# Kernel optimization log

Hardware: AMD Instinct MI355X
Metric: run time of the kernel (lower is better)

## Reference

```python
import jax, jax.numpy as jnp
import numpy as np

D = 1024       # d_model
H = 16         # num_heads
DK = D // H    # head dim (64)
DFF = 4096     # SwiGLU hidden dim
THETA = 10000.0
EPS = 1e-5
B, S = 2, 2048


def setup_inputs() -> dict:
    key = jax.random.key(0)
    ks = jax.random.split(key, 9)
    p = lambda k, shape: jax.random.normal(k, shape, dtype=jnp.float32) * 0.02
    return {
        "x": jax.random.normal(ks[0], (B, S, D), dtype=jnp.float32),
        "w_q": p(ks[1], (D, D)),   # Linear stores [out, in]
        "w_k": p(ks[2], (D, D)),
        "w_v": p(ks[3], (D, D)),
        "w_o": p(ks[4], (D, D)),
        "ln1_w": jnp.ones((D,), dtype=jnp.float32),
        "ln2_w": jnp.ones((D,), dtype=jnp.float32),
        "w1": p(ks[5], (DFF, D)),  # gate-in proj: d_model -> dff
        "w2": p(ks[6], (D, DFF)),  # down proj:    dff -> d_model
        "w3": p(ks[7], (DFF, D)),  # up proj:      d_model -> dff
    }


def _rmsnorm(x, w):
    xf = x.astype(jnp.float32)
    inv = jax.lax.rsqrt(jnp.mean(xf * xf, axis=-1, keepdims=True) + EPS)
    return (inv * xf * w).astype(x.dtype)


def _rope(x, pos):
    # x: [..., seq, DK]; pos: [seq]
    inv_freq = THETA ** (-(jnp.arange(0, DK, 2, dtype=jnp.float32) / DK))  # [DK/2]
    ang = pos.astype(jnp.float32)[:, None] * inv_freq                      # [seq, DK/2]
    cos, sin = jnp.cos(ang), jnp.sin(ang)
    xe, xo = x[..., ::2], x[..., 1::2]
    re = cos * xe - sin * xo
    ro = sin * xe + cos * xo
    return jnp.stack((re, ro), axis=-1).reshape(x.shape)  # interleave even/odd


def reference(x, w_q, w_k, w_v, w_o, ln1_w, ln2_w, w1, w2, w3):
    b, s, d = x.shape
    pos = jnp.arange(s)

    # --- attention sublayer ---
    h = _rmsnorm(x, ln1_w)
    def proj(w):  # [b,s,d] x [d,d] -> [b,H,s,DK]
        return jnp.einsum('bsd,ed->bse', h, w).reshape(b, s, H, DK).transpose(0, 2, 1, 3)
    q = _rope(proj(w_q), pos)
    k = _rope(proj(w_k), pos)
    v = proj(w_v)

    scores = jnp.einsum('bhqd,bhkd->bhqk', q, k) / (DK ** 0.5)
    causal = jnp.tril(jnp.ones((s, s), dtype=bool))
    scores = jnp.where(causal, scores, -jnp.inf)
    attn = jax.nn.softmax(scores, axis=-1)
    o = jnp.einsum('bhqk,bhkd->bhqd', attn, v).transpose(0, 2, 1, 3).reshape(b, s, d)
    x = x + jnp.einsum('bsd,ed->bse', o, w_o)

    # --- SwiGLU FFN sublayer ---
    h2 = _rmsnorm(x, ln2_w)
    u = jnp.einsum('bsd,fd->bsf', h2, w1)
    g = jnp.einsum('bsd,fd->bsf', h2, w3)
    ffn = jnp.einsum('bsf,df->bsd', u * jax.nn.sigmoid(u) * g, w2)
    return x + ffn
```

## Files before the change

### kernel.cpp

```cpp
#include <hip/hip_runtime.h>

typedef _Float16 half_t;
typedef _Float16 f16x8 __attribute__((ext_vector_type(8)));
typedef _Float16 f16x4 __attribute__((ext_vector_type(4)));
typedef _Float16 f16x2 __attribute__((ext_vector_type(2)));
typedef float fx4 __attribute__((ext_vector_type(4)));

typedef __attribute__((address_space(1))) const unsigned int as1_cuint;
typedef __attribute__((address_space(3))) unsigned int as3_uint;

__device__ __forceinline__ void gld16(const void* g, void* l) {
    __builtin_amdgcn_global_load_lds((as1_cuint*)g, (as3_uint*)l, 16, 0, 0);
}

#define L256(buf, half, sec) (lbase + (buf) * 65536 + (half) * 16384 + (sec) * 8192)

#define KT256(CUR)                                                            \
  {                                                                           \
    const int BO = (CUR) * 65536;                                             \
    const int st1 = (t < nt - 1), st2 = (t < nt - 2);                         \
    const int s1 = (t + 1) * 128, s2 = (t + 2) * 128;                         \
    f16x8 aLo[4][2], aHi[4][2], bA[2][2], bB[2][2];                           \
                                         \
    _Pragma("unroll") for (int mi = 0; mi < 4; mi++) {                        \
        aLo[mi][0] = *(const f16x8*)(aBase + BO + mi * 2048 + swz0);          \
        aLo[mi][1] = *(const f16x8*)(aBase + BO + mi * 2048 + swz1);          \
    }                                                                         \
    _Pragma("unroll") for (int ni = 0; ni < 2; ni++) {                        \
        bA[ni][0] = *(const f16x8*)(bBase + BO + ni * 2048 + swz0);           \
        bA[ni][1] = *(const f16x8*)(bBase + BO + ni * 2048 + swz1);           \
    }                                                                         \
    if (st1) { gld16(pB10 + s1, L256(1 - (CUR), 3, 0));                       \
               gld16(pB1h + s1, L256(1 - (CUR), 3, 1)); }                     \
    asm volatile("s_waitcnt lgkmcnt(8)" ::: "memory");                        \
    __builtin_amdgcn_s_barrier();                                             \
    asm volatile("s_waitcnt lgkmcnt(0)" ::: "memory");                        \
    __builtin_amdgcn_sched_barrier(0);                                        \
    __builtin_amdgcn_s_setprio(1);                                            \
    _Pragma("unroll") for (int kk = 0; kk < 2; kk++)                          \
      _Pragma("unroll") for (int mi = 0; mi < 4; mi++)                        \
        _Pragma("unroll") for (int ni = 0; ni < 2; ni++)                      \
          acc[mi][ni] = __builtin_amdgcn_mfma_f32_16x16x32_f16(aLo[mi][kk], bA[ni][kk], acc[mi][ni], 0, 0, 0); \
    __builtin_amdgcn_s_setprio(0);                                            \
    __builtin_amdgcn_s_barrier();                                             \
                                         \
    _Pragma("unroll") for (int ni = 0; ni < 2; ni++) {                        \
        bB[ni][0] = *(const f16x8*)(bBase + BO + (2 + ni) * 2048 + swz0);     \
        bB[ni][1] = *(const f16x8*)(bBase + BO + (2 + ni) * 2048 + swz1);     \
    }                                                                         \
    if (st2) { gld16(pA00 + s2, L256(CUR, 0, 0)); }                           \
    __builtin_amdgcn_s_barrier();                                             \
    asm volatile("s_waitcnt lgkmcnt(0)" ::: "memory");                        \
    __builtin_amdgcn_sched_barrier(0);                                        \
    __builtin_amdgcn_s_setprio(1);                                            \
    _Pragma("unroll") for (int kk = 0; kk < 2; kk++)                          \
      _Pragma("unroll") for (int mi = 0; mi < 4; mi++)                        \
        _Pragma("unroll") for (int ni = 0; ni < 2; ni++)                      \
          acc[mi][2 + ni] = __builtin_amdgcn_mfma_f32_16x16x32_f16(aLo[mi][kk], bB[ni][kk], acc[mi][2 + ni], 0, 0, 0); \
    __builtin_amdgcn_s_setprio(0);                                            \
    __builtin_amdgcn_s_barrier();                                             \
                                         \
    _Pragma("unroll") for (int mi = 0; mi < 4; mi++) {                        \
        aHi[mi][0] = *(const f16x8*)(aBase + BO + (4 + mi) * 2048 + swz0);    \
        aHi[mi][1] = *(const f16x8*)(aBase + BO + (4 + mi) * 2048 + swz1);    \
    }                                                                         \
    if (st2) { gld16(pB00 + s2, L256(CUR, 2, 0));                             \
               gld16(pB0h + s2, L256(CUR, 2, 1)); }                           \
    __builtin_amdgcn_s_barrier();                                             \
    asm volatile("s_waitcnt lgkmcnt(0)" ::: "memory");                        \
    __builtin_amdgcn_sched_barrier(0);                                        \
    __builtin_amdgcn_s_setprio(1);                                            \
    _Pragma("unroll") for (int kk = 0; kk < 2; kk++)                          \
      _Pragma("unroll") for (int mi = 0; mi < 4; mi++)                        \
        _Pragma("unroll") for (int ni = 0; ni < 2; ni++)                      \
          acc[4 + mi][2 + ni] = __builtin_amdgcn_mfma_f32_16x16x32_f16(aHi[mi][kk], bB[ni][kk], acc[4 + mi][2 + ni], 0, 0, 0); \
    __builtin_amdgcn_s_setprio(0);                                            \
    __builtin_amdgcn_s_barrier();                                             \
                                         \
    if (st2) { gld16(pA0h + s2, L256(CUR, 0, 1));                             \
               gld16(pA10 + s2, L256(CUR, 1, 0));                             \
               gld16(pA1h + s2, L256(CUR, 1, 1)); }                           \
    __builtin_amdgcn_s_barrier();                                             \
    __builtin_amdgcn_sched_barrier(0);                                        \
    __builtin_amdgcn_s_setprio(1);                                            \
    _Pragma("unroll") for (int kk = 0; kk < 2; kk++)                          \
      _Pragma("unroll") for (int mi = 0; mi < 4; mi++)                        \
        _Pragma("unroll") for (int ni = 0; ni < 2; ni++)                      \
          acc[4 + mi][ni] = __builtin_amdgcn_mfma_f32_16x16x32_f16(aHi[mi][kk], bA[ni][kk], acc[4 + mi][ni], 0, 0, 0); \
    __builtin_amdgcn_s_setprio(0);                                            \
    if (t < nt - 2)       { asm volatile("s_waitcnt vmcnt(6)" ::: "memory"); }\
    else if (t == nt - 2) { asm volatile("s_waitcnt vmcnt(0)" ::: "memory"); }\
    __builtin_amdgcn_s_barrier();                                             \
  }

template<int MODE>
__global__ __launch_bounds__(512, 2)
void gemm256(const half_t* __restrict__ A,
             const half_t* __restrict__ B0, const half_t* __restrict__ B1,
             const half_t* __restrict__ B2,
             half_t* o0, half_t* o1, half_t* o2, half_t* o3,
             int M, int N, int K)
{
    __shared__ half_t smem[65536];
    const int tid = threadIdx.x;
    const int wid = tid >> 6, lane = tid & 63;
    const int lm = lane & 15, lg = lane >> 4;
    const int wr = wid >> 2, wc = wid & 3;
    const int m0 = blockIdx.x * 256, n0 = blockIdx.y * 256;

    const half_t* Bp = B0;
    half_t* outb = o0;
    if (MODE == 1) {
        if (blockIdx.z == 1) { Bp = B1; outb = o1; }
        else if (blockIdx.z == 2) { Bp = B2; outb = o2; }
    }
    if (MODE == 4) {
        if (blockIdx.z == 1) outb = o1;
        else if (blockIdx.z == 2) outb = o2;
        else if (blockIdx.z == 3) outb = o3;
    }
    int Keff = K, koff = 0;
    if (MODE == 4) { Keff = K / gridDim.z; koff = blockIdx.z * Keff; }
    const int nt = Keff >> 6;

    const size_t KB = (size_t)K * 2;
    const int srow = tid >> 3;
    const int schunk = (tid & 7) ^ (srow & 7);
    const char* pA = (const char*)A + (size_t)(m0 + srow) * KB + (size_t)koff * 2 + schunk * 16;
    const char* pB = (const char*)Bp + (size_t)(n0 + srow) * KB + (size_t)koff * 2 + schunk * 16;
    const char* pA00 = pA;
    const char* pA0h = pA + 64 * KB;
    const char* pA10 = pA + 128 * KB;
    const char* pA1h = pA + 192 * KB;
    const char* pB00 = pB;
    const char* pB0h = pB + 64 * KB;
    const char* pB10 = pB + 128 * KB;
    const char* pB1h = pB + 192 * KB;

    char* const lbase = (char*)smem + tid * 16;

    const int swz0 = ((lg ^ (lm & 7)) << 4);
    const int swz1 = (((4 + lg) ^ (lm & 7)) << 4);
    const char* aBase = (const char*)smem + wr * 16384 + lm * 128;
    const char* bBase = (const char*)smem + (2 + (wc >> 1)) * 16384 + (wc & 1) * 8192 + lm * 128;

    gld16(pA00, L256(0, 0, 0));
    gld16(pB00, L256(0, 2, 0)); gld16(pB0h, L256(0, 2, 1));
    gld16(pA0h, L256(0, 0, 1)); gld16(pA10, L256(0, 1, 0)); gld16(pA1h, L256(0, 1, 1));
    gld16(pB10, L256(0, 3, 0)); gld16(pB1h, L256(0, 3, 1));
    gld16(pA00 + 128, L256(1, 0, 0));
    gld16(pB00 + 128, L256(1, 2, 0)); gld16(pB0h + 128, L256(1, 2, 1));
    gld16(pA0h + 128, L256(1, 0, 1)); gld16(pA10 + 128, L256(1, 1, 0)); gld16(pA1h + 128, L256(1, 1, 1));
    asm volatile("s_waitcnt vmcnt(6)" ::: "memory");
    __builtin_amdgcn_s_barrier();

    fx4 acc[8][4] = {};

#pragma unroll 1
    for (int tt = 0; tt < nt; tt += 2) {
        { const int t = tt;     KT256(0) }
        { const int t = tt + 1; KT256(1) }
    }

#pragma unroll
    for (int mi = 0; mi < 8; mi++) {
#pragma unroll
        for (int ni = 0; ni < 4; ni++) {
#pragma unroll
            for (int r = 0; r < 4; r++) {
                int m = m0 + wr * 128 + mi * 16 + lg * 4 + r;
                int n = n0 + wc * 64 + ni * 16 + lm;
                float v = acc[mi][ni][r];
                if (MODE == 1) {
                    int b = m >> 11, s = m & 2047, hh = n >> 6, dk = n & 63;
                    if (blockIdx.z == 2) {
                        outb[((size_t)(b * 16 + hh) * 64 + dk) * 2048 + s] = (half_t)v;
                    } else {
                        outb[((size_t)(b * 16 + hh) * 2048 + s) * 64 + dk] = (half_t)v;
                    }
                } else {
                    outb[(size_t)m * N + n] = (half_t)v;
                }
            }
        }
    }
}

__global__ __launch_bounds__(512, 2)
void gemm_dual9(const half_t* __restrict__ A,
                const half_t* __restrict__ B1, const half_t* __restrict__ B2,
                half_t* __restrict__ out, int M, int N, int K)
{
    __shared__ half_t smem[65536];
    const int tid = threadIdx.x;
    const int wid = tid >> 6, lane = tid & 63;
    const int lm = lane & 15, lg = lane >> 4;
    const int wr = wid >> 2, wc = wid & 3;
    const int m0 = blockIdx.x * 256, n0 = blockIdx.y * 128;

    const size_t KB = (size_t)K * 2;
    const int srow = tid >> 3;
    const int schunk = (tid & 7) ^ (srow & 7);
    const char* pA  = (const char*)A  + (size_t)(m0 + srow) * KB + schunk * 16;
    const char* pB0 = (const char*)B1 + (size_t)(n0 + srow) * KB + schunk * 16;
    const char* pB1 = (const char*)B2 + (size_t)(n0 + srow) * KB + schunk * 16;
    const char* pA00 = pA;
    const char* pA0h = pA + 64 * KB;
    const char* pA10 = pA + 128 * KB;
    const char* pA1h = pA + 192 * KB;
    const char* pB0h = pB0 + 64 * KB;
    const char* pB1h = pB1 + 64 * KB;

    char* const lbase = (char*)smem + tid * 16;

    const int lA = lm * 128;
    const int swz0 = ((lg ^ (lm & 7)) << 4);
    const int swz1 = (((4 + lg) ^ (lm & 7)) << 4);
    const char* aBase = (const char*)smem + wr * 16384 + lA;
    const char* bBase = (const char*)smem + (2 + (wc >> 1)) * 16384 + (wc & 1) * 8192 + lA;

    gld16(pA00, L256(0, 0, 0));
    gld16(pB0,  L256(0, 2, 0)); gld16(pB0h, L256(0, 2, 1));
    gld16(pA0h, L256(0, 0, 1)); gld16(pA10, L256(0, 1, 0)); gld16(pA1h, L256(0, 1, 1));
    gld16(pB1,  L256(0, 3, 0)); gld16(pB1h, L256(0, 3, 1));
    gld16(pA00 + 128, L256(1, 0, 0));
    gld16(pB0 + 128,  L256(1, 2, 0)); gld16(pB0h + 128, L256(1, 2, 1));
    gld16(pA0h + 128, L256(1, 0, 1)); gld16(pA10 + 128, L256(1, 1, 0)); gld16(pA1h + 128, L256(1, 1, 1));
    asm volatile("s_waitcnt vmcnt(6)" ::: "memory");
    __builtin_amdgcn_s_barrier();

    fx4 acc[8][4] = {};

#pragma unroll
    for (int t = 0; t < 16; ++t) {
        const int BO = (t & 1) * 65536;
        const int s1 = (t + 1) * 128, s2 = (t + 2) * 128;
        const int b1 = (t + 1) & 1, b2 = t & 1;
        f16x8 aLo[4][2], aHi[4][2], bA[2][2], bB[2][2];

#pragma unroll
        for (int mi = 0; mi < 4; mi++) {
            aLo[mi][0] = *(const f16x8*)(aBase + BO + mi * 2048 + swz0);
            aLo[mi][1] = *(const f16x8*)(aBase + BO + mi * 2048 + swz1);
        }
#pragma unroll
        for (int ni = 0; ni < 2; ni++) {
            bA[ni][0] = *(const f16x8*)(bBase + BO + ni * 2048 + swz0);
            bA[ni][1] = *(const f16x8*)(bBase + BO + ni * 2048 + swz1);
        }
        if (t < 15) { gld16(pB1 + s1, L256(b1, 3, 0)); gld16(pB1h + s1, L256(b1, 3, 1)); }
        asm volatile("s_waitcnt lgkmcnt(8)" ::: "memory");
        __builtin_amdgcn_s_barrier();
        asm volatile("s_waitcnt lgkmcnt(0)" ::: "memory");
        __builtin_amdgcn_sched_barrier(0);
        __builtin_amdgcn_s_setprio(1);
#pragma unroll
        for (int kk = 0; kk < 2; kk++)
#pragma unroll
            for (int mi = 0; mi < 4; mi++)
#pragma unroll
                for (int ni = 0; ni < 2; ni++)
                    acc[mi][ni] = __builtin_amdgcn_mfma_f32_16x16x32_f16(aLo[mi][kk], bA[ni][kk], acc[mi][ni], 0, 0, 0);
        __builtin_amdgcn_s_setprio(0);
        __builtin_amdgcn_s_barrier();

#pragma unroll
        for (int ni = 0; ni < 2; ni++) {
            bB[ni][0] = *(const f16x8*)(bBase + BO + (2 + ni) * 2048 + swz0);
            bB[ni][1] = *(const f16x8*)(bBase + BO + (2 + ni) * 2048 + swz1);
        }
        if (t < 14) { gld16(pA00 + s2, L256(b2, 0, 0)); }
        __builtin_amdgcn_s_barrier();
        asm volatile("s_waitcnt lgkmcnt(0)" ::: "memory");
        __builtin_amdgcn_sched_barrier(0);
        __builtin_amdgcn_s_setprio(1);
#pragma unroll
        for (int kk = 0; kk < 2; kk++)
#pragma unroll
            for (int mi = 0; mi < 4; mi++)
#pragma unroll
                for (int ni = 0; ni < 2; ni++)
                    acc[mi][2 + ni] = __builtin_amdgcn_mfma_f32_16x16x32_f16(aLo[mi][kk], bB[ni][kk], acc[mi][2 + ni], 0, 0, 0);
        __builtin_amdgcn_s_setprio(0);
        __builtin_amdgcn_s_barrier();

#pragma unroll
        for (int mi = 0; mi < 4; mi++) {
            aHi[mi][0] = *(const f16x8*)(aBase + BO + (4 + mi) * 2048 + swz0);
            aHi[mi][1] = *(const f16x8*)(aBase + BO + (4 + mi) * 2048 + swz1);
        }
        if (t < 14) { gld16(pB0 + s2, L256(b2, 2, 0)); gld16(pB0h + s2, L256(b2, 2, 1)); }
        __builtin_amdgcn_s_barrier();
        asm volatile("s_waitcnt lgkmcnt(0)" ::: "memory");
        __builtin_amdgcn_sched_barrier(0);
        __builtin_amdgcn_s_setprio(1);
#pragma unroll
        for (int kk = 0; kk < 2; kk++)
#pragma unroll
            for (int mi = 0; mi < 4; mi++)
#pragma unroll
                for (int ni = 0; ni < 2; ni++)
                    acc[4 + mi][2 + ni] = __builtin_amdgcn_mfma_f32_16x16x32_f16(aHi[mi][kk], bB[ni][kk], acc[4 + mi][2 + ni], 0, 0, 0);
        __builtin_amdgcn_s_setprio(0);
        __builtin_amdgcn_s_barrier();

        if (t < 14) {
            gld16(pA0h + s2, L256(b2, 0, 1));
            gld16(pA10 + s2, L256(b2, 1, 0));
            gld16(pA1h + s2, L256(b2, 1, 1));
        }
        __builtin_amdgcn_s_barrier();
        __builtin_amdgcn_sched_barrier(0);
        __builtin_amdgcn_s_setprio(1);
#pragma unroll
        for (int kk = 0; kk < 2; kk++)
#pragma unroll
            for (int mi = 0; mi < 4; mi++)
#pragma unroll
                for (int ni = 0; ni < 2; ni++)
                    acc[4 + mi][ni] = __builtin_amdgcn_mfma_f32_16x16x32_f16(aHi[mi][kk], bA[ni][kk], acc[4 + mi][ni], 0, 0, 0);
        __builtin_amdgcn_s_setprio(0);
        if (t < 14)      { asm volatile("s_waitcnt vmcnt(6)" ::: "memory"); }
        else if (t == 14){ asm volatile("s_waitcnt vmcnt(0)" ::: "memory"); }
        __builtin_amdgcn_s_barrier();
    }

    float* gb = (float*)smem;
    if (wc >= 2) {
        const int gw = wr * 2 + (wc - 2);
#pragma unroll
        for (int mi = 0; mi < 8; mi++)
#pragma unroll
            for (int ni = 0; ni < 4; ni++)
                *(fx4*)((char*)gb + ((((gw * 8 + mi) * 4 + ni) * 64 + lane) << 4)) = acc[mi][ni];
    }
    __syncthreads();
    if (wc < 2) {
        const int gw = wr * 2 + wc;
#pragma unroll
        for (int mi = 0; mi < 8; mi++)
#pragma unroll
            for (int ni = 0; ni < 4; ni++) {
                fx4 gv = *(const fx4*)((const char*)gb + ((((gw * 8 + mi) * 4 + ni) * 64 + lane) << 4));
#pragma unroll
                for (int r = 0; r < 4; r++) {
                    int m = m0 + wr * 128 + mi * 16 + lg * 4 + r;
                    int n = n0 + wc * 64 + ni * 16 + lm;
                    float u = acc[mi][ni][r], g = gv[r];
                    out[(size_t)m * N + n] = (half_t)(u / (1.f + __expf(-u)) * g);
                }
            }
    }
}

__global__ __launch_bounds__(256, 4)
void addnorm_k(const float* __restrict__ x,
               const half_t* __restrict__ p0, const half_t* __restrict__ p1,
               const half_t* __restrict__ p2, const half_t* __restrict__ p3,
               const float* __restrict__ w,
               float* __restrict__ outF, half_t* __restrict__ outH)
{
    int row = blockIdx.x * 4 + (threadIdx.x >> 6);
    int lane = threadIdx.x & 63;
    const float4* xr = (const float4*)(x + (size_t)row * 1024);
    const f16x4* p0r = (const f16x4*)(p0 + (size_t)row * 1024);
    const f16x4* p1r = (const f16x4*)(p1 + (size_t)row * 1024);
    const f16x4* p2r = (const f16x4*)(p2 + (size_t)row * 1024);
    const f16x4* p3r = (const f16x4*)(p3 + (size_t)row * 1024);
    float4 v[4];
    float s = 0.f;
#pragma unroll
    for (int i = 0; i < 4; i++) {
        float4 xv = xr[lane + 64 * i];
        f16x4 a0 = p0r[lane + 64 * i];
        f16x4 a1 = p1r[lane + 64 * i];
        f16x4 a2 = p2r[lane + 64 * i];
        f16x4 a3 = p3r[lane + 64 * i];
        v[i].x = xv.x + (float)a0[0] + (float)a1[0] + (float)a2[0] + (float)a3[0];
        v[i].y = xv.y + (float)a0[1] + (float)a1[1] + (float)a2[1] + (float)a3[1];
        v[i].z = xv.z + (float)a0[2] + (float)a1[2] + (float)a2[2] + (float)a3[2];
        v[i].w = xv.w + (float)a0[3] + (float)a1[3] + (float)a2[3] + (float)a3[3];
        s += v[i].x * v[i].x + v[i].y * v[i].y + v[i].z * v[i].z + v[i].w * v[i].w;
    }
#pragma unroll
    for (int o = 32; o > 0; o >>= 1) s += __shfl_xor(s, o);
    float inv = rsqrtf(s * (1.f / 1024.f) + 1e-5f);
    const float4* w4 = (const float4*)w;
    float4* oF = (float4*)(outF + (size_t)row * 1024);
    f16x4* oH = (f16x4*)(outH + (size_t)row * 1024);
#pragma unroll
    for (int i = 0; i < 4; i++) {
        oF[lane + 64 * i] = v[i];
        float4 wv = w4[lane + 64 * i];
        f16x4 ov = { (half_t)(v[i].x * inv * wv.x), (half_t)(v[i].y * inv * wv.y),
                     (half_t)(v[i].z * inv * wv.z), (half_t)(v[i].w * inv * wv.w) };
        oH[lane + 64 * i] = ov;
    }
}

__global__ __launch_bounds__(256, 8)
void reduce4_k(const half_t* __restrict__ p0, const half_t* __restrict__ p1,
               const half_t* __restrict__ p2, const half_t* __restrict__ p3,
               float* __restrict__ out, int n4)
{
    int i = blockIdx.x * 256 + threadIdx.x;
    if (i >= n4) return;
    float4 b = ((const float4*)out)[i];
    f16x4 a0 = ((const f16x4*)p0)[i];
    f16x4 a1 = ((const f16x4*)p1)[i];
    f16x4 a2 = ((const f16x4*)p2)[i];
    f16x4 a3 = ((const f16x4*)p3)[i];
    float4 o = { b.x + (float)a0[0] + (float)a1[0] + (float)a2[0] + (float)a3[0],
                 b.y + (float)a0[1] + (float)a1[1] + (float)a2[1] + (float)a3[1],
                 b.z + (float)a0[2] + (float)a1[2] + (float)a2[2] + (float)a3[2],
                 b.w + (float)a0[3] + (float)a1[3] + (float)a2[3] + (float)a3[3] };
    ((float4*)out)[i] = o;
}

__global__ __launch_bounds__(256, 4)
void rmsnorm_k(const float* __restrict__ x, const float* __restrict__ w,
               half_t* __restrict__ out)
{
    int row = blockIdx.x * 4 + (threadIdx.x >> 6);
    int lane = threadIdx.x & 63;
    const float4* xr = (const float4*)(x + (size_t)row * 1024);
    float4 v[4];
    float s = 0.f;
#pragma unroll
    for (int i = 0; i < 4; i++) {
        v[i] = xr[lane + 64 * i];
        s += v[i].x * v[i].x + v[i].y * v[i].y + v[i].z * v[i].z + v[i].w * v[i].w;
    }
#pragma unroll
    for (int o = 32; o > 0; o >>= 1) s += __shfl_xor(s, o);
    float inv = rsqrtf(s * (1.f / 1024.f) + 1e-5f);
    const float4* w4 = (const float4*)w;
    f16x4* o4 = (f16x4*)(out + (size_t)row * 1024);
#pragma unroll
    for (int i = 0; i < 4; i++) {
        float4 wv = w4[lane + 64 * i];
        f16x4 ov = { (half_t)(v[i].x * inv * wv.x), (half_t)(v[i].y * inv * wv.y),
                     (half_t)(v[i].z * inv * wv.z), (half_t)(v[i].w * inv * wv.w) };
        o4[lane + 64 * i] = ov;
    }
}

struct CastA { const float* s; half_t* d; int n4; };
struct CastArgs { CastA a[7]; };

__global__ void cast_k(CastArgs ca)
{
    CastA a = ca.a[blockIdx.y];
    int i = blockIdx.x * 256 + threadIdx.x;
    if (i >= a.n4) return;
    float4 v = ((const float4*)a.s)[i];
    ((f16x4*)a.d)[i] = (f16x4){ (half_t)v.x, (half_t)v.y, (half_t)v.z, (half_t)v.w };
}

__global__ void rope_k(half_t* Q, half_t* Kv)
{
    int idx = blockIdx.x * 256 + threadIdx.x;
    half_t* P = blockIdx.y ? Kv : Q;
    float scq = blockIdx.y ? 1.0f : 0.125f;
    int i = idx & 31;
    int s = (idx >> 5) & 2047;
    int bh = idx >> 16;
    float f = __expf((float)i * -0.28782313662f);
    float ang = (float)s * f;
    float c = cosf(ang), sn = sinf(ang);
    f16x2* p = (f16x2*)(P + ((size_t)bh * 2048 + s) * 64 + 2 * i);
    f16x2 xv = *p;
    float xe = (float)xv[0], xo = (float)xv[1];
    *p = (f16x2){ (half_t)((c * xe - sn * xo) * scq), (half_t)((sn * xe + c * xo) * scq) };
}

__global__ __launch_bounds__(256, 2)
void attn_k(const half_t* __restrict__ Q, const half_t* __restrict__ K,
            const half_t* __restrict__ VT, half_t* __restrict__ O)
{
    __shared__ half_t sK[128 * 64];
    __shared__ half_t sVT[64 * 128];
    __shared__ half_t sP[4][16 * 128];
    const int tid = threadIdx.x, wid = tid >> 6, lane = tid & 63;
    const int lm = lane & 15, lg = lane >> 4;
    const int p = blockIdx.x, bh = blockIdx.y;
    const int b = bh >> 4, hh = bh & 15;
    const size_t base = (size_t)bh * (2048 * 64);

    const int krow = tid >> 3;
    const int kcsw = ((tid & 7) ^ (krow & 7)) << 4;
    const int vrow = tid >> 4;
    const int vcsw = ((tid & 15) ^ (vrow & 15)) << 4;
    const char* gK = (const char*)(K + base);
    const char* gV = (const char*)(VT + base);
    char* lK = (char*)sK + tid * 16;
    char* lV = (char*)sVT + tid * 16;
    half_t* sPw = sP[wid];

    f16x8 vone;
#pragma unroll
    for (int j = 0; j < 8; j++) vone[j] = (half_t)1.f;

    for (int ph = 0; ph < 2; ph++) {
        const int qt = ph ? (31 - p) : p;
        const int q0 = qt * 64 + wid * 16;
        const int nT = (qt + 2) >> 1;

        f16x8 bQ[2];
#pragma unroll
        for (int ki = 0; ki < 2; ki++)
            bQ[ki] = *(const f16x8*)(Q + base + (size_t)(q0 + lm) * 64 + ki * 32 + lg * 8);

        fx4 oacc[4] = {};
        fx4 lacc = {};

        for (int t = 0; t < nT; t++) {
            const int kv0 = t * 128;
#pragma unroll
            for (int i = 0; i < 4; i++)
                gld16(gK + (size_t)(kv0 + i * 32 + krow) * 128 + kcsw, lK + i * 4096);
#pragma unroll
            for (int i = 0; i < 4; i++)
                gld16(gV + (size_t)(i * 16 + vrow) * 4096 + (size_t)kv0 * 2 + vcsw, lV + i * 4096);
            __syncthreads();

            fx4 st[8] = {};
#pragma unroll
            for (int ki = 0; ki < 2; ki++) {
#pragma unroll
                for (int mi = 0; mi < 8; mi++) {
                    f16x8 aK = *(const f16x8*)(sK + ((mi * 16 + lm) << 6) +
                                               (((ki * 4 + lg) ^ (lm & 7)) << 3));
                    st[mi] = __builtin_amdgcn_mfma_f32_16x16x32_f16(aK, bQ[ki], st[mi], 0, 0, 0);
                }
            }

            const bool diag = (t == nT - 1);
            const int qg = q0 + lm;
#pragma unroll
            for (int mi = 0; mi < 8; mi++) {
                f16x4 ev;
#pragma unroll
                for (int r = 0; r < 4; r++) {
                    float e = __expf(st[mi][r]);
                    if (diag && (kv0 + mi * 16 + lg * 4 + r > qg)) e = 0.f;
                    ev[r] = (half_t)e;
                }
                *(f16x4*)(sPw + (lm << 7) +
                          ((((mi * 2 + (lg >> 1)) ^ lm) << 3) | ((lg & 1) << 2))) = ev;
            }

#pragma unroll
            for (int k2 = 0; k2 < 4; k2++) {
                f16x8 aP = *(const f16x8*)(sPw + (lm << 7) + (((k2 * 4 + lg) ^ lm) << 3));
#pragma unroll
                for (int ni = 0; ni < 4; ni++) {
                    f16x8 bV = *(const f16x8*)(sVT + ((ni * 16 + lm) << 7) +
                                               (((k2 * 4 + lg) ^ lm) << 3));
                    oacc[ni] = __builtin_amdgcn_mfma_f32_16x16x32_f16(aP, bV, oacc[ni], 0, 0, 0);
                }
                lacc = __builtin_amdgcn_mfma_f32_16x16x32_f16(aP, vone, lacc, 0, 0, 0);
            }
            __syncthreads();
        }

        float inv[4];
#pragma unroll
        for (int r = 0; r < 4; r++) inv[r] = 1.f / lacc[r];
#pragma unroll
        for (int ni = 0; ni < 4; ni++)
#pragma unroll
            for (int r = 0; r < 4; r++) {
                int s = q0 + lg * 4 + r;
                O[((size_t)b * 2048 + s) * 1024 + hh * 64 + ni * 16 + lm] =
                    (half_t)(oacc[ni][r] * inv[r]);
            }
    }
}

extern "C" void kernel_launch(void* const* d_in, const int* in_sizes, int n_in,
                              void* d_out, int out_size, void* d_ws, size_t ws_size,
                              hipStream_t stream)
{
    const float* x   = (const float*)d_in[0];
    const float* wq  = (const float*)d_in[1];
    const float* wk  = (const float*)d_in[2];
    const float* wv  = (const float*)d_in[3];
    const float* wo  = (const float*)d_in[4];
    const float* ln1 = (const float*)d_in[5];
    const float* ln2 = (const float*)d_in[6];
    const float* w1  = (const float*)d_in[7];
    const float* w2  = (const float*)d_in[8];
    const float* w3  = (const float*)d_in[9];

    half_t* W = (half_t*)d_ws;
    const size_t Mi = 1048576;
    half_t* wq16 = W;
    half_t* wk16 = W + Mi;
    half_t* wv16 = W + 2 * Mi;
    half_t* wo16 = W + 3 * Mi;
    half_t* w116 = W + 4 * Mi;
    half_t* w316 = W + 8 * Mi;
    half_t* w216 = W + 12 * Mi;
    half_t* h16  = W + 16 * Mi;
    half_t* q16  = W + 20 * Mi;
    half_t* k16  = W + 24 * Mi;
    half_t* vt16 = W + 28 * Mi;
    half_t* a16  = W + 16 * Mi;
    half_t* h216 = W + 32 * Mi;
    half_t* P0   = W + 20 * Mi;
    half_t* P1   = W + 24 * Mi;
    half_t* P2   = W + 28 * Mi;
    half_t* P3   = W + 36 * Mi;
    half_t* D0   = W;
    half_t* D1   = W + 4 * Mi;
    half_t* D2   = W + 8 * Mi;
    half_t* D3   = W + 36 * Mi;

    CastArgs ca;
    ca.a[0] = { wq, wq16, 262144 };
    ca.a[1] = { wk, wk16, 262144 };
    ca.a[2] = { wv, wv16, 262144 };
    ca.a[3] = { wo, wo16, 262144 };
    ca.a[4] = { w1, w116, 1048576 };
    ca.a[5] = { w2, w216, 1048576 };
    ca.a[6] = { w3, w316, 1048576 };

    cast_k<<<dim3(4096, 7), 256, 0, stream>>>(ca);
    rmsnorm_k<<<dim3(1024), 256, 0, stream>>>(x, ln1, h16);
    gemm256<1><<<dim3(16, 4, 3), 512, 0, stream>>>(h16, wq16, wk16, wv16,
                                                   q16, k16, vt16, nullptr,
                                                   4096, 1024, 1024);
    rope_k<<<dim3(8192, 2), 256, 0, stream>>>(q16, k16);
    attn_k<<<dim3(16, 32), 256, 0, stream>>>(q16, k16, vt16, h16);
    gemm256<4><<<dim3(16, 4, 4), 512, 0, stream>>>(h16, wo16, nullptr, nullptr,
                                                   P0, P1, P2, P3,
                                                   4096, 1024, 1024);
    addnorm_k<<<dim3(1024), 256, 0, stream>>>(x, P0, P1, P2, P3, ln2,
                                              (float*)d_out, h216);
    gemm_dual9<<<dim3(16, 32), 512, 0, stream>>>(h216, w116, w316, a16,
                                                 4096, 4096, 1024);
    gemm256<4><<<dim3(16, 4, 4), 512, 0, stream>>>(a16, w216, nullptr, nullptr,
                                                   D0, D1, D2, D3,
                                                   4096, 1024, 4096);
    reduce4_k<<<dim3(4096), 256, 0, stream>>>(D0, D1, D2, D3, (float*)d_out, 1048576);
    (void)in_sizes; (void)n_in; (void)out_size; (void)ws_size;
}
```

Baseline: 398.9 us.

## Fuse RoPE into QKV epilogue, merge cast+rmsnorm, remap blocks, reuse KT256 in dual GEMM

```diff
diff --git a/kernel.cpp b/kernel.cpp
--- a/kernel.cpp
+++ b/kernel.cpp
@@ -93,6 +93,17 @@
     __builtin_amdgcn_s_barrier();                                             \
   }
 
+#define PRO256()                                                              \
+    gld16(pA00, L256(0, 0, 0));                                               \
+    gld16(pB00, L256(0, 2, 0)); gld16(pB0h, L256(0, 2, 1));                   \
+    gld16(pA0h, L256(0, 0, 1)); gld16(pA10, L256(0, 1, 0)); gld16(pA1h, L256(0, 1, 1)); \
+    gld16(pB10, L256(0, 3, 0)); gld16(pB1h, L256(0, 3, 1));                   \
+    gld16(pA00 + 128, L256(1, 0, 0));                                         \
+    gld16(pB00 + 128, L256(1, 2, 0)); gld16(pB0h + 128, L256(1, 2, 1));       \
+    gld16(pA0h + 128, L256(1, 0, 1)); gld16(pA10 + 128, L256(1, 1, 0)); gld16(pA1h + 128, L256(1, 1, 1)); \
+    asm volatile("s_waitcnt vmcnt(6)" ::: "memory");                          \
+    __builtin_amdgcn_s_barrier();
+
 template<int MODE>
 __global__ __launch_bounds__(512, 2)
 void gemm256(const half_t* __restrict__ A,
@@ -144,15 +155,7 @@
     const char* aBase = (const char*)smem + wr * 16384 + lm * 128;
     const char* bBase = (const char*)smem + (2 + (wc >> 1)) * 16384 + (wc & 1) * 8192 + lm * 128;
 
-    gld16(pA00, L256(0, 0, 0));
-    gld16(pB00, L256(0, 2, 0)); gld16(pB0h, L256(0, 2, 1));
-    gld16(pA0h, L256(0, 0, 1)); gld16(pA10, L256(0, 1, 0)); gld16(pA1h, L256(0, 1, 1));
-    gld16(pB10, L256(0, 3, 0)); gld16(pB1h, L256(0, 3, 1));
-    gld16(pA00 + 128, L256(1, 0, 0));
-    gld16(pB00 + 128, L256(1, 2, 0)); gld16(pB0h + 128, L256(1, 2, 1));
-    gld16(pA0h + 128, L256(1, 0, 1)); gld16(pA10 + 128, L256(1, 1, 0)); gld16(pA1h + 128, L256(1, 1, 1));
-    asm volatile("s_waitcnt vmcnt(6)" ::: "memory");
-    __builtin_amdgcn_s_barrier();
+    PRO256()
 
     fx4 acc[8][4] = {};
 
@@ -176,7 +179,15 @@
                     if (blockIdx.z == 2) {
                         outb[((size_t)(b * 16 + hh) * 64 + dk) * 2048 + s] = (half_t)v;
                     } else {
-                        outb[((size_t)(b * 16 + hh) * 2048 + s) * 64 + dk] = (half_t)v;
+                        float pv = __shfl_xor(v, 1);
+                        float f = __expf((float)(dk >> 1) * -0.28782313662f);
+                        float c, sn;
+                        __sincosf((float)s * f, &sn, &c);
+                        float xe = (lm & 1) ? pv : v;
+                        float xo = (lm & 1) ? v : pv;
+                        float rv = (lm & 1) ? (sn * xe + c * xo) : (c * xe - sn * xo);
+                        if (blockIdx.z == 0) rv *= 0.125f;
+                        outb[((size_t)(b * 16 + hh) * 2048 + s) * 64 + dk] = (half_t)rv;
                     }
                 } else {
                     outb[(size_t)m * N + n] = (half_t)v;
@@ -196,7 +207,9 @@
     const int wid = tid >> 6, lane = tid & 63;
     const int lm = lane & 15, lg = lane >> 4;
     const int wr = wid >> 2, wc = wid & 3;
-    const int m0 = blockIdx.x * 256, n0 = blockIdx.y * 128;
+    const int flat = blockIdx.x + (blockIdx.y << 4);
+    const int wg = (flat & 7) * 64 + (flat >> 3);
+    const int m0 = (wg & 15) * 256, n0 = (wg >> 4) * 128;
 
     const size_t KB = (size_t)K * 2;
     const int srow = tid >> 3;
@@ -208,121 +221,27 @@
     const char* pA0h = pA + 64 * KB;
     const char* pA10 = pA + 128 * KB;
     const char* pA1h = pA + 192 * KB;
+    const char* pB00 = pB0;
     const char* pB0h = pB0 + 64 * KB;
+    const char* pB10 = pB1;
     const char* pB1h = pB1 + 64 * KB;
+    const int nt = 16;
 
     char* const lbase = (char*)smem + tid * 16;
 
-    const int lA = lm * 128;
     const int swz0 = ((lg ^ (lm & 7)) << 4);
     const int swz1 = (((4 + lg) ^ (lm & 7)) << 4);
-    const char* aBase = (const char*)smem + wr * 16384 + lA;
-    const char* bBase = (const char*)smem + (2 + (wc >> 1)) * 16384 + (wc & 1) * 8192 + lA;
-
-    gld16(pA00, L256(0, 0, 0));
-    gld16(pB0,  L256(0, 2, 0)); gld16(pB0h, L256(0, 2, 1));
-    gld16(pA0h, L256(0, 0, 1)); gld16(pA10, L256(0, 1, 0)); gld16(pA1h, L256(0, 1, 1));
-    gld16(pB1,  L256(0, 3, 0)); gld16(pB1h, L256(0, 3, 1));
-    gld16(pA00 + 128, L256(1, 0, 0));
-    gld16(pB0 + 128,  L256(1, 2, 0)); gld16(pB0h + 128, L256(1, 2, 1));
-    gld16(pA0h + 128, L256(1, 0, 1)); gld16(pA10 + 128, L256(1, 1, 0)); gld16(pA1h + 128, L256(1, 1, 1));
-    asm volatile("s_waitcnt vmcnt(6)" ::: "memory");
-    __builtin_amdgcn_s_barrier();
+    const char* aBase = (const char*)smem + wr * 16384 + lm * 128;
+    const char* bBase = (const char*)smem + (2 + (wc >> 1)) * 16384 + (wc & 1) * 8192 + lm * 128;
+
+    PRO256()
 
     fx4 acc[8][4] = {};
 
-#pragma unroll
-    for (int t = 0; t < 16; ++t) {
-        const int BO = (t & 1) * 65536;
-        const int s1 = (t + 1) * 128, s2 = (t + 2) * 128;
-        const int b1 = (t + 1) & 1, b2 = t & 1;
-        f16x8 aLo[4][2], aHi[4][2], bA[2][2], bB[2][2];
-
-#pragma unroll
-        for (int mi = 0; mi < 4; mi++) {
-            aLo[mi][0] = *(const f16x8*)(aBase + BO + mi * 2048 + swz0);
-            aLo[mi][1] = *(const f16x8*)(aBase + BO + mi * 2048 + swz1);
-        }
-#pragma unroll
-        for (int ni = 0; ni < 2; ni++) {
-            bA[ni][0] = *(const f16x8*)(bBase + BO + ni * 2048 + swz0);
-            bA[ni][1] = *(const f16x8*)(bBase + BO + ni * 2048 + swz1);
-        }
-        if (t < 15) { gld16(pB1 + s1, L256(b1, 3, 0)); gld16(pB1h + s1, L256(b1, 3, 1)); }
-        asm volatile("s_waitcnt lgkmcnt(8)" ::: "memory");
-        __builtin_amdgcn_s_barrier();
-        asm volatile("s_waitcnt lgkmcnt(0)" ::: "memory");
-        __builtin_amdgcn_sched_barrier(0);
-        __builtin_amdgcn_s_setprio(1);
-#pragma unroll
-        for (int kk = 0; kk < 2; kk++)
-#pragma unroll
-            for (int mi = 0; mi < 4; mi++)
-#pragma unroll
-                for (int ni = 0; ni < 2; ni++)
-                    acc[mi][ni] = __builtin_amdgcn_mfma_f32_16x16x32_f16(aLo[mi][kk], bA[ni][kk], acc[mi][ni], 0, 0, 0);
-        __builtin_amdgcn_s_setprio(0);
-        __builtin_amdgcn_s_barrier();
-
-#pragma unroll
-        for (int ni = 0; ni < 2; ni++) {
-            bB[ni][0] = *(const f16x8*)(bBase + BO + (2 + ni) * 2048 + swz0);
-            bB[ni][1] = *(const f16x8*)(bBase + BO + (2 + ni) * 2048 + swz1);
-        }
-        if (t < 14) { gld16(pA00 + s2, L256(b2, 0, 0)); }
-        __builtin_amdgcn_s_barrier();
-        asm volatile("s_waitcnt lgkmcnt(0)" ::: "memory");
-        __builtin_amdgcn_sched_barrier(0);
-        __builtin_amdgcn_s_setprio(1);
-#pragma unroll
-        for (int kk = 0; kk < 2; kk++)
-#pragma unroll
-            for (int mi = 0; mi < 4; mi++)
-#pragma unroll
-                for (int ni = 0; ni < 2; ni++)
-                    acc[mi][2 + ni] = __builtin_amdgcn_mfma_f32_16x16x32_f16(aLo[mi][kk], bB[ni][kk], acc[mi][2 + ni], 0, 0, 0);
-        __builtin_amdgcn_s_setprio(0);
-        __builtin_amdgcn_s_barrier();
-
-#pragma unroll
-        for (int mi = 0; mi < 4; mi++) {
-            aHi[mi][0] = *(const f16x8*)(aBase + BO + (4 + mi) * 2048 + swz0);
-            aHi[mi][1] = *(const f16x8*)(aBase + BO + (4 + mi) * 2048 + swz1);
-        }
-        if (t < 14) { gld16(pB0 + s2, L256(b2, 2, 0)); gld16(pB0h + s2, L256(b2, 2, 1)); }
-        __builtin_amdgcn_s_barrier();
-        asm volatile("s_waitcnt lgkmcnt(0)" ::: "memory");
-        __builtin_amdgcn_sched_barrier(0);
-        __builtin_amdgcn_s_setprio(1);
-#pragma unroll
-        for (int kk = 0; kk < 2; kk++)
-#pragma unroll
-            for (int mi = 0; mi < 4; mi++)
-#pragma unroll
-                for (int ni = 0; ni < 2; ni++)
-                    acc[4 + mi][2 + ni] = __builtin_amdgcn_mfma_f32_16x16x32_f16(aHi[mi][kk], bB[ni][kk], acc[4 + mi][2 + ni], 0, 0, 0);
-        __builtin_amdgcn_s_setprio(0);
-        __builtin_amdgcn_s_barrier();
-
-        if (t < 14) {
-            gld16(pA0h + s2, L256(b2, 0, 1));
-            gld16(pA10 + s2, L256(b2, 1, 0));
-            gld16(pA1h + s2, L256(b2, 1, 1));
-        }
-        __builtin_amdgcn_s_barrier();
-        __builtin_amdgcn_sched_barrier(0);
-        __builtin_amdgcn_s_setprio(1);
-#pragma unroll
-        for (int kk = 0; kk < 2; kk++)
-#pragma unroll
-            for (int mi = 0; mi < 4; mi++)
-#pragma unroll
-                for (int ni = 0; ni < 2; ni++)
-                    acc[4 + mi][ni] = __builtin_amdgcn_mfma_f32_16x16x32_f16(aHi[mi][kk], bA[ni][kk], acc[4 + mi][ni], 0, 0, 0);
-        __builtin_amdgcn_s_setprio(0);
-        if (t < 14)      { asm volatile("s_waitcnt vmcnt(6)" ::: "memory"); }
-        else if (t == 14){ asm volatile("s_waitcnt vmcnt(0)" ::: "memory"); }
-        __builtin_amdgcn_s_barrier();
+#pragma unroll 1
+    for (int tt = 0; tt < 16; tt += 2) {
+        { const int t = tt;     KT256(0) }
+        { const int t = tt + 1; KT256(1) }
     }
 
     float* gb = (float*)smem;
@@ -417,10 +336,22 @@
     ((float4*)out)[i] = o;
 }
 
-__global__ __launch_bounds__(256, 4)
-void rmsnorm_k(const float* __restrict__ x, const float* __restrict__ w,
-               half_t* __restrict__ out)
-{
+struct CastA { const float* s; half_t* d; int n4; };
+struct CastArgs { CastA a[7]; };
+
+__global__ __launch_bounds__(256)
+void cast_rms_k(CastArgs ca, const float* __restrict__ x,
+                const float* __restrict__ w, half_t* __restrict__ out)
+{
+    if (blockIdx.y < 7) {
+        CastA a = ca.a[blockIdx.y];
+        int i = blockIdx.x * 256 + threadIdx.x;
+        if (i >= a.n4) return;
+        float4 v = ((const float4*)a.s)[i];
+        ((f16x4*)a.d)[i] = (f16x4){ (half_t)v.x, (half_t)v.y, (half_t)v.z, (half_t)v.w };
+        return;
+    }
+    if (blockIdx.x >= 1024) return;
     int row = blockIdx.x * 4 + (threadIdx.x >> 6);
     int lane = threadIdx.x & 63;
     const float4* xr = (const float4*)(x + (size_t)row * 1024);
@@ -445,35 +376,6 @@
     }
 }
 
-struct CastA { const float* s; half_t* d; int n4; };
-struct CastArgs { CastA a[7]; };
-
-__global__ void cast_k(CastArgs ca)
-{
-    CastA a = ca.a[blockIdx.y];
-    int i = blockIdx.x * 256 + threadIdx.x;
-    if (i >= a.n4) return;
-    float4 v = ((const float4*)a.s)[i];
-    ((f16x4*)a.d)[i] = (f16x4){ (half_t)v.x, (half_t)v.y, (half_t)v.z, (half_t)v.w };
-}
-
-__global__ void rope_k(half_t* Q, half_t* Kv)
-{
-    int idx = blockIdx.x * 256 + threadIdx.x;
-    half_t* P = blockIdx.y ? Kv : Q;
-    float scq = blockIdx.y ? 1.0f : 0.125f;
-    int i = idx & 31;
-    int s = (idx >> 5) & 2047;
-    int bh = idx >> 16;
-    float f = __expf((float)i * -0.28782313662f);
-    float ang = (float)s * f;
-    float c = cosf(ang), sn = sinf(ang);
-    f16x2* p = (f16x2*)(P + ((size_t)bh * 2048 + s) * 64 + 2 * i);
-    f16x2 xv = *p;
-    float xe = (float)xv[0], xo = (float)xv[1];
-    *p = (f16x2){ (half_t)((c * xe - sn * xo) * scq), (half_t)((sn * xe + c * xo) * scq) };
-}
-
 __global__ __launch_bounds__(256, 2)
 void attn_k(const half_t* __restrict__ Q, const half_t* __restrict__ K,
             const half_t* __restrict__ VT, half_t* __restrict__ O)
@@ -483,7 +385,9 @@
     __shared__ half_t sP[4][16 * 128];
     const int tid = threadIdx.x, wid = tid >> 6, lane = tid & 63;
     const int lm = lane & 15, lg = lane >> 4;
-    const int p = blockIdx.x, bh = blockIdx.y;
+    const int flat = blockIdx.x + (blockIdx.y << 4);
+    const int wg = (flat & 7) * 64 + (flat >> 3);
+    const int p = wg & 15, bh = wg >> 4;
     const int b = bh >> 4, hh = bh & 15;
     const size_t base = (size_t)bh * (2048 * 64);
 
@@ -626,12 +530,10 @@
     ca.a[5] = { w2, w216, 1048576 };
     ca.a[6] = { w3, w316, 1048576 };
 
-    cast_k<<<dim3(4096, 7), 256, 0, stream>>>(ca);
-    rmsnorm_k<<<dim3(1024), 256, 0, stream>>>(x, ln1, h16);
+    cast_rms_k<<<dim3(4096, 8), 256, 0, stream>>>(ca, x, ln1, h16);
     gemm256<1><<<dim3(16, 4, 3), 512, 0, stream>>>(h16, wq16, wk16, wv16,
                                                    q16, k16, vt16, nullptr,
                                                    4096, 1024, 1024);
-    rope_k<<<dim3(8192, 2), 256, 0, stream>>>(q16, k16);
     attn_k<<<dim3(16, 32), 256, 0, stream>>>(q16, k16, vt16, h16);
     gemm256<4><<<dim3(16, 4, 4), 512, 0, stream>>>(h16, wo16, nullptr, nullptr,
                                                    P0, P1, P2, P3,
```

Result: faster. 388.9 us (-2.5%).
